# Optimization experiments

Measured on AMD Instinct MI355X. Metric: run time of the kernel, lower is better.

Reference implementation:

```python
import jax, jax.numpy as jnp
import numpy as np


def setup_inputs() -> dict:
    key = jax.random.key(0)
    k1, k2 = jax.random.split(key)
    B, H, W, D = 4096, 64, 64, 512
    inputs = jax.random.normal(k1, (B, D), dtype=jnp.float32)
    # keras 'random_uniform' initializer default range [-0.05, 0.05]
    weights_map = jax.random.uniform(k2, (H, W, D), dtype=jnp.float32,
                                     minval=-0.05, maxval=0.05)
    return {"inputs": inputs, "weights_map": weights_map}


def reference(inputs, weights_map):
    # inputs: (B, D); weights_map: (H, W, D)
    H, W, D = weights_map.shape
    flat_w = weights_map.reshape(-1, D)              # (N, D), N = H*W
    # avoids materializing the (B, N, D) difference tensor)
    x_sq = jnp.sum(inputs * inputs, axis=1, keepdims=True)    # (B, 1)
    w_sq = jnp.sum(flat_w * flat_w, axis=1)                   # (N,)
    sq_dist = x_sq - 2.0 * (inputs @ flat_w.T) + w_sq         # (B, N)
    sq_dist = jnp.maximum(sq_dist, 0.0)
    bmu_flat = jnp.argmin(sq_dist, axis=1)                    # (B,)
    bmu_y = (bmu_flat // W).astype(jnp.int32)
    bmu_x = (bmu_flat % W).astype(jnp.int32)
    bmu_indices = jnp.stack([bmu_y, bmu_x], axis=1)           # (B, 2)
    min_sq = jnp.take_along_axis(sq_dist, bmu_flat[:, None], axis=1)[:, 0]
    quantization_errors = jnp.sqrt(min_sq)                    # (B,)
    return bmu_indices, quantization_errors
```

## Files before the change

### kernel.cpp

```cpp
#include <hip/hip_runtime.h>

#define B_ROWS 4096
#define N_COLS 4096
#define DIM    512
#define LDK    1024

typedef __attribute__((ext_vector_type(8))) short short8;
typedef __attribute__((ext_vector_type(4))) float floatx4;

__device__ __forceinline__ unsigned short f2bf_rn(float f) {
    unsigned u = __float_as_uint(f);
    u += 0x7fffu + ((u >> 16) & 1u);
    return (unsigned short)(u >> 16);
}
__device__ __forceinline__ float bf2f(unsigned short h) {
    return __uint_as_float(((unsigned)h) << 16);
}

__device__ __forceinline__ unsigned long long pack_key(float v, int idx) {
    unsigned u = __float_as_uint(v);
    u = (u & 0x80000000u) ? ~u : (u | 0x80000000u);
    return ((unsigned long long)u << 32) | (unsigned)idx;
}

__device__ __forceinline__ void async16(const unsigned short* g, unsigned short* l) {
    __builtin_amdgcn_global_load_lds(
        (__attribute__((address_space(1))) void*)g,
        (__attribute__((address_space(3))) void*)l, 16, 0, 0);
}

__global__ __launch_bounds__(256) void som_convert(
    const float* __restrict__ X, const float* __restrict__ Wt,
    unsigned short* __restrict__ Xc, unsigned short* __restrict__ Wc,
    float* __restrict__ x_sq, float* __restrict__ w_sq,
    unsigned long long* __restrict__ packed)
{
    int wave = threadIdx.x >> 6, lane = threadIdx.x & 63;
    int grow = blockIdx.x * 4 + wave;
    bool isX = grow < B_ROWS;
    const float* src = isX ? (X + (size_t)grow * DIM)
                           : (Wt + (size_t)(grow - B_ROWS) * DIM);
    const float4* p4 = (const float4*)src;
    float4 a = p4[lane * 2], b = p4[lane * 2 + 1];
    float f[8] = {a.x, a.y, a.z, a.w, b.x, b.y, b.z, b.w};
    unsigned short hi[8], lo[8];
    float s = 0.f;
    #pragma unroll
    for (int t = 0; t < 8; ++t) {
        hi[t] = f2bf_rn(f[t]);
        lo[t] = f2bf_rn(f[t] - bf2f(hi[t]));
        s = fmaf(f[t], f[t], s);
    }
    unsigned short* dst = (isX ? Xc + (size_t)grow * LDK
                               : Wc + (size_t)(grow - B_ROWS) * LDK) + lane * 8;
    *(ushort4*)(dst)       = make_ushort4(hi[0], hi[1], hi[2], hi[3]);
    *(ushort4*)(dst + 4)   = make_ushort4(hi[4], hi[5], hi[6], hi[7]);
    *(ushort4*)(dst + 512) = make_ushort4(lo[0], lo[1], lo[2], lo[3]);
    *(ushort4*)(dst + 516) = make_ushort4(lo[4], lo[5], lo[6], lo[7]);
    #pragma unroll
    for (int off = 32; off >= 1; off >>= 1) s += __shfl_xor(s, off, 64);
    if (lane == 0) {
        if (isX) { x_sq[grow] = s; packed[grow] = ~0ull; }
        else     { w_sq[grow - B_ROWS] = s; }
    }
}

__global__ __launch_bounds__(256, 3) void som_dist_bf16(
    const unsigned short* __restrict__ Xc, const unsigned short* __restrict__ Wc,
    const float* __restrict__ w_sq, unsigned long long* __restrict__ packed)
{
    __shared__ unsigned short Ah[128 * 32];
    __shared__ unsigned short Al[128 * 32];
    __shared__ unsigned short Bh[128 * 32];
    __shared__ unsigned short Bl[128 * 32];
    const int tid  = threadIdx.x;
    const int wave = tid >> 6, lane = tid & 63;
    const int wr = wave >> 1, wc = wave & 1;
    const int bm = blockIdx.y, bn = blockIdx.x;
    const int quad = lane >> 4, t16 = lane & 15;

    const int srow = lane >> 2;
    const int scol = (lane & 3) * 8;
    const unsigned short* gAh = Xc + (size_t)(bm * 128 + wave * 32 + srow) * LDK + scol;
    const unsigned short* gBh = Wc + (size_t)(bn * 128 + wave * 32 + srow) * LDK + scol;
    const unsigned short* gAl = gAh + 512;
    const unsigned short* gBl = gBh + 512;
    unsigned short* lAh = &Ah[(wave * 32) * 32];
    unsigned short* lAl = &Al[(wave * 32) * 32];
    unsigned short* lBh = &Bh[(wave * 32) * 32];
    unsigned short* lBl = &Bl[(wave * 32) * 32];

    const unsigned short* pah = &Ah[(wr * 64 + t16) * 32 + quad * 8];
    const unsigned short* pal = &Al[(wr * 64 + t16) * 32 + quad * 8];
    const unsigned short* pbh = &Bh[(wc * 64 + t16) * 32 + quad * 8];
    const unsigned short* pbl = &Bl[(wc * 64 + t16) * 32 + quad * 8];

    floatx4 acc[4][4];
    #pragma unroll
    for (int i = 0; i < 4; ++i)
        #pragma unroll
        for (int j = 0; j < 4; ++j) acc[i][j] = (floatx4){0.f, 0.f, 0.f, 0.f};

    #pragma unroll 1
    for (int k0 = 0; k0 < DIM; k0 += 32) {
        __syncthreads();
        async16(gAh + k0,            lAh);
        async16(gAh + k0 + 16 * LDK, lAh + 16 * 32);
        async16(gAl + k0,            lAl);
        async16(gAl + k0 + 16 * LDK, lAl + 16 * 32);
        async16(gBh + k0,            lBh);
        async16(gBh + k0 + 16 * LDK, lBh + 16 * 32);
        async16(gBl + k0,            lBl);
        async16(gBl + k0 + 16 * LDK, lBl + 16 * 32);
        __syncthreads();

        short8 ah[4], bh[4], x[4];
        #pragma unroll
        for (int i = 0; i < 4; ++i) ah[i] = *(const short8*)(pah + i * 16 * 32);
        #pragma unroll
        for (int j = 0; j < 4; ++j) bh[j] = *(const short8*)(pbh + j * 16 * 32);
        #pragma unroll
        for (int i = 0; i < 4; ++i)
            #pragma unroll
            for (int j = 0; j < 4; ++j)
                acc[i][j] = __builtin_amdgcn_mfma_f32_16x16x32_bf16(
                    ah[i], bh[j], acc[i][j], 0, 0, 0);

        #pragma unroll
        for (int j = 0; j < 4; ++j) x[j] = *(const short8*)(pbl + j * 16 * 32);
        #pragma unroll
        for (int i = 0; i < 4; ++i)
            #pragma unroll
            for (int j = 0; j < 4; ++j)
                acc[i][j] = __builtin_amdgcn_mfma_f32_16x16x32_bf16(
                    ah[i], x[j], acc[i][j], 0, 0, 0);

        #pragma unroll
        for (int i = 0; i < 4; ++i) x[i] = *(const short8*)(pal + i * 16 * 32);
        #pragma unroll
        for (int i = 0; i < 4; ++i)
            #pragma unroll
            for (int j = 0; j < 4; ++j)
                acc[i][j] = __builtin_amdgcn_mfma_f32_16x16x32_bf16(
                    x[i], bh[j], acc[i][j], 0, 0, 0);
    }

    const int col0 = bn * 128 + wc * 64 + t16;
    float wq[4];
    #pragma unroll
    for (int j = 0; j < 4; ++j) wq[j] = w_sq[col0 + j * 16];
    const int row_base = bm * 128 + wr * 64 + quad * 4;
    #pragma unroll
    for (int i = 0; i < 4; ++i) {
        #pragma unroll
        for (int r = 0; r < 4; ++r) {
            unsigned long long best = ~0ull;
            #pragma unroll
            for (int j = 0; j < 4; ++j) {
                float val = fmaf(-2.f, acc[i][j][r], wq[j]);
                unsigned long long key = pack_key(val, col0 + j * 16);
                best = (key < best) ? key : best;
            }
            #pragma unroll
            for (int m = 1; m <= 8; m <<= 1) {
                unsigned long long o = __shfl_xor(best, m, 64);
                best = (o < best) ? o : best;
            }
            if (t16 == 0)
                atomicMin(&packed[row_base + i * 16 + r], best);
        }
    }
}

__global__ __launch_bounds__(256) void som_finalize(
    const unsigned long long* __restrict__ packed,
    const float* __restrict__ x_sq, float* __restrict__ out)
{
    int b = blockIdx.x * 256 + threadIdx.x;
    unsigned long long p = packed[b];
    unsigned idx = (unsigned)(p & 0xffffffffull);
    unsigned key = (unsigned)(p >> 32);
    unsigned u = (key & 0x80000000u) ? (key & 0x7fffffffu) : ~key;
    float val = __uint_as_float(u);
    float sq = fmaxf(x_sq[b] + val, 0.f);
    out[2 * b]     = (float)(idx >> 6);
    out[2 * b + 1] = (float)(idx & 63);
    out[2 * B_ROWS + b] = sqrtf(sq);
}

extern "C" void kernel_launch(void* const* d_in, const int* in_sizes, int n_in,
                              void* d_out, int out_size, void* d_ws, size_t ws_size,
                              hipStream_t stream) {
    const float* X  = (const float*)d_in[0];
    const float* Wt = (const float*)d_in[1];
    float* out = (float*)d_out;

    unsigned long long* packed = (unsigned long long*)d_ws;
    float* x_sq = (float*)((char*)d_ws + (32 << 10));
    float* w_sq = (float*)((char*)d_ws + (48 << 10));
    unsigned short* Xc = (unsigned short*)((char*)d_ws + (64 << 10));
    unsigned short* Wc = (unsigned short*)((char*)d_ws + (64 << 10) + ((size_t)B_ROWS * LDK * 2));

    som_convert<<<dim3((B_ROWS + N_COLS) / 4), dim3(256), 0, stream>>>(
        X, Wt, Xc, Wc, x_sq, w_sq, packed);
    som_dist_bf16<<<dim3(N_COLS / 128, B_ROWS / 128), dim3(256), 0, stream>>>(
        Xc, Wc, w_sq, packed);
    som_finalize<<<dim3(B_ROWS / 256), dim3(256), 0, stream>>>(packed, x_sq, out);
}
```

Baseline: 124.3 us.

## Enlarge GEMM tile to 256x256 with double-buffered LDS and 8 waves

Replaces the 128x128, 4-wave distance GEMM with a 256x256 block tile run by 8 waves, each owning a 128x64 output sub-tile. LDS is double-buffered, so global-to-LDS async loads for the next K slice overlap MFMA work on the current one, with one barrier per iteration instead of two. Raising MFMA priority with s_setprio is meant to favour compute issue. The costs are more accumulator registers (128 floats per lane), 128 KB of LDS per block, and only 256 blocks in the grid, which may leave some CUs idle or lower occupancy.

```diff
diff --git a/kernel.cpp b/kernel.cpp
--- a/kernel.cpp
+++ b/kernel.cpp
@@ -65,93 +65,103 @@
     }
 }
 
-__global__ __launch_bounds__(256, 3) void som_dist_bf16(
+__global__ __launch_bounds__(512, 2) void som_dist_v2(
     const unsigned short* __restrict__ Xc, const unsigned short* __restrict__ Wc,
     const float* __restrict__ w_sq, unsigned long long* __restrict__ packed)
 {
-    __shared__ unsigned short Ah[128 * 32];
-    __shared__ unsigned short Al[128 * 32];
-    __shared__ unsigned short Bh[128 * 32];
-    __shared__ unsigned short Bl[128 * 32];
+    __shared__ __align__(16) unsigned short L[2 * 64 * 512];
     const int tid  = threadIdx.x;
     const int wave = tid >> 6, lane = tid & 63;
-    const int wr = wave >> 1, wc = wave & 1;
+    const int quad = lane >> 4, t16 = lane & 15;
+    const int wr = wave >> 2, wc = wave & 3;
     const int bm = blockIdx.y, bn = blockIdx.x;
-    const int quad = lane >> 4, t16 = lane & 15;
-
-    const int srow = lane >> 2;
-    const int scol = (lane & 3) * 8;
-    const unsigned short* gAh = Xc + (size_t)(bm * 128 + wave * 32 + srow) * LDK + scol;
-    const unsigned short* gBh = Wc + (size_t)(bn * 128 + wave * 32 + srow) * LDK + scol;
-    const unsigned short* gAl = gAh + 512;
-    const unsigned short* gBl = gBh + 512;
-    unsigned short* lAh = &Ah[(wave * 32) * 32];
-    unsigned short* lAl = &Al[(wave * 32) * 32];
-    unsigned short* lBh = &Bh[(wave * 32) * 32];
-    unsigned short* lBl = &Bl[(wave * 32) * 32];
-
-    const unsigned short* pah = &Ah[(wr * 64 + t16) * 32 + quad * 8];
-    const unsigned short* pal = &Al[(wr * 64 + t16) * 32 + quad * 8];
-    const unsigned short* pbh = &Bh[(wc * 64 + t16) * 32 + quad * 8];
-    const unsigned short* pbl = &Bl[(wc * 64 + t16) * 32 + quad * 8];
-
-    floatx4 acc[4][4];
-    #pragma unroll
-    for (int i = 0; i < 4; ++i)
+
+    const int sg = wave & 3;
+    const bool stB = (wave >= 4);
+    const unsigned short* gsrc =
+        (stB ? Wc + (size_t)bn * 256 * LDK : Xc + (size_t)bm * 256 * LDK)
+        + (size_t)(sg * 64 + t16) * LDK + quad * 8;
+    unsigned short* const lwav = &L[(stB ? 16384 : 0) + sg * 4096];
+
+    const unsigned short* const pA = &L[wr * 8192 + lane * 8];
+    const unsigned short* const pB = &L[16384 + wc * 4096 + lane * 8];
+
+    floatx4 acc[8][4];
+    #pragma unroll
+    for (int i = 0; i < 8; ++i)
         #pragma unroll
         for (int j = 0; j < 4; ++j) acc[i][j] = (floatx4){0.f, 0.f, 0.f, 0.f};
 
-    #pragma unroll 1
-    for (int k0 = 0; k0 < DIM; k0 += 32) {
-        __syncthreads();
-        async16(gAh + k0,            lAh);
-        async16(gAh + k0 + 16 * LDK, lAh + 16 * 32);
-        async16(gAl + k0,            lAl);
-        async16(gAl + k0 + 16 * LDK, lAl + 16 * 32);
-        async16(gBh + k0,            lBh);
-        async16(gBh + k0 + 16 * LDK, lBh + 16 * 32);
-        async16(gBl + k0,            lBl);
-        async16(gBl + k0 + 16 * LDK, lBl + 16 * 32);
-        __syncthreads();
-
-        short8 ah[4], bh[4], x[4];
-        #pragma unroll
-        for (int i = 0; i < 4; ++i) ah[i] = *(const short8*)(pah + i * 16 * 32);
-        #pragma unroll
-        for (int j = 0; j < 4; ++j) bh[j] = *(const short8*)(pbh + j * 16 * 32);
-        #pragma unroll
-        for (int i = 0; i < 4; ++i)
+    #pragma unroll
+    for (int q = 0; q < 4; ++q) {
+        async16(gsrc + q * 16 * LDK,       lwav + q * 1024);
+        async16(gsrc + q * 16 * LDK + 512, lwav + q * 1024 + 512);
+    }
+    __syncthreads();
+
+    #pragma unroll 2
+    for (int kt = 0; kt < 16; ++kt) {
+        const int cur = kt & 1;
+        const unsigned short* pAc = pA + cur * 32768;
+        const unsigned short* pBc = pB + cur * 32768;
+
+        if (kt < 15) {
+            const unsigned short* gs = gsrc + (kt + 1) * 32;
+            unsigned short* ld = lwav + (cur ^ 1) * 32768;
+            #pragma unroll
+            for (int q = 0; q < 4; ++q) {
+                async16(gs + q * 16 * LDK,       ld + q * 1024);
+                async16(gs + q * 16 * LDK + 512, ld + q * 1024 + 512);
+            }
+        }
+
+        short8 ah[8], bh[4], x4[4];
+        #pragma unroll
+        for (int i = 0; i < 8; ++i) ah[i] = *(const short8*)(pAc + i * 1024);
+        #pragma unroll
+        for (int j = 0; j < 4; ++j) bh[j] = *(const short8*)(pBc + j * 1024);
+        __builtin_amdgcn_s_setprio(1);
+        #pragma unroll
+        for (int i = 0; i < 8; ++i)
             #pragma unroll
             for (int j = 0; j < 4; ++j)
                 acc[i][j] = __builtin_amdgcn_mfma_f32_16x16x32_bf16(
                     ah[i], bh[j], acc[i][j], 0, 0, 0);
-
-        #pragma unroll
-        for (int j = 0; j < 4; ++j) x[j] = *(const short8*)(pbl + j * 16 * 32);
-        #pragma unroll
-        for (int i = 0; i < 4; ++i)
+        __builtin_amdgcn_s_setprio(0);
+
+        #pragma unroll
+        for (int j = 0; j < 4; ++j) x4[j] = *(const short8*)(pBc + j * 1024 + 512);
+        __builtin_amdgcn_s_setprio(1);
+        #pragma unroll
+        for (int i = 0; i < 8; ++i)
             #pragma unroll
             for (int j = 0; j < 4; ++j)
                 acc[i][j] = __builtin_amdgcn_mfma_f32_16x16x32_bf16(
-                    ah[i], x[j], acc[i][j], 0, 0, 0);
-
-        #pragma unroll
-        for (int i = 0; i < 4; ++i) x[i] = *(const short8*)(pal + i * 16 * 32);
-        #pragma unroll
-        for (int i = 0; i < 4; ++i)
+                    ah[i], x4[j], acc[i][j], 0, 0, 0);
+        __builtin_amdgcn_s_setprio(0);
+
+        short8 al[8];
+        #pragma unroll
+        for (int i = 0; i < 8; ++i) al[i] = *(const short8*)(pAc + i * 1024 + 512);
+        __builtin_amdgcn_s_setprio(1);
+        #pragma unroll
+        for (int i = 0; i < 8; ++i)
             #pragma unroll
             for (int j = 0; j < 4; ++j)
                 acc[i][j] = __builtin_amdgcn_mfma_f32_16x16x32_bf16(
-                    x[i], bh[j], acc[i][j], 0, 0, 0);
-    }
-
-    const int col0 = bn * 128 + wc * 64 + t16;
+                    al[i], bh[j], acc[i][j], 0, 0, 0);
+        __builtin_amdgcn_s_setprio(0);
+
+        __syncthreads();
+    }
+
+    const int col0 = bn * 256 + wc * 64 + t16;
     float wq[4];
     #pragma unroll
     for (int j = 0; j < 4; ++j) wq[j] = w_sq[col0 + j * 16];
-    const int row_base = bm * 128 + wr * 64 + quad * 4;
-    #pragma unroll
-    for (int i = 0; i < 4; ++i) {
+    const int row_base = bm * 256 + wr * 128 + quad * 4;
+    #pragma unroll
+    for (int i = 0; i < 8; ++i) {
         #pragma unroll
         for (int r = 0; r < 4; ++r) {
             unsigned long long best = ~0ull;
@@ -203,7 +213,7 @@
 
     som_convert<<<dim3((B_ROWS + N_COLS) / 4), dim3(256), 0, stream>>>(
         X, Wt, Xc, Wc, x_sq, w_sq, packed);
-    som_dist_bf16<<<dim3(N_COLS / 128, B_ROWS / 128), dim3(256), 0, stream>>>(
+    som_dist_v2<<<dim3(N_COLS / 256, B_ROWS / 256), dim3(512), 0, stream>>>(
         Xc, Wc, w_sq, packed);
     som_finalize<<<dim3(B_ROWS / 256), dim3(256), 0, stream>>>(packed, x_sq, out);
 }
```

After: 118.7 us. -4.5%, faster.

## Reorganize LDS tile layout, remap blocks per XCD, widen convert stores

Applied to the files above, without the earlier changes.

The LDS tiles are laid out so that each MFMA operand fragment sits contiguously per lane (lane*8). This aims to cut bank conflicts on the short8 LDS reads. Global-to-LDS loads are split so waves 0-1 stage X and waves 2-3 stage W, with hi and lo halves interleaved per fragment. Block IDs are remapped so that blocks sharing an XCD work on neighbouring bm/bn tiles, improving L2 reuse. The convert kernel now writes 16-byte short8 stores instead of 8-byte ones.

```diff
diff --git a/kernel.cpp b/kernel.cpp
--- a/kernel.cpp
+++ b/kernel.cpp
@@ -43,20 +43,19 @@
     const float4* p4 = (const float4*)src;
     float4 a = p4[lane * 2], b = p4[lane * 2 + 1];
     float f[8] = {a.x, a.y, a.z, a.w, b.x, b.y, b.z, b.w};
-    unsigned short hi[8], lo[8];
+    short8 hi, lo;
     float s = 0.f;
     #pragma unroll
     for (int t = 0; t < 8; ++t) {
-        hi[t] = f2bf_rn(f[t]);
-        lo[t] = f2bf_rn(f[t] - bf2f(hi[t]));
+        unsigned short h = f2bf_rn(f[t]);
+        hi[t] = (short)h;
+        lo[t] = (short)f2bf_rn(f[t] - bf2f(h));
         s = fmaf(f[t], f[t], s);
     }
     unsigned short* dst = (isX ? Xc + (size_t)grow * LDK
                                : Wc + (size_t)(grow - B_ROWS) * LDK) + lane * 8;
-    *(ushort4*)(dst)       = make_ushort4(hi[0], hi[1], hi[2], hi[3]);
-    *(ushort4*)(dst + 4)   = make_ushort4(hi[4], hi[5], hi[6], hi[7]);
-    *(ushort4*)(dst + 512) = make_ushort4(lo[0], lo[1], lo[2], lo[3]);
-    *(ushort4*)(dst + 516) = make_ushort4(lo[4], lo[5], lo[6], lo[7]);
+    *(short8*)(dst)       = hi;
+    *(short8*)(dst + 512) = lo;
     #pragma unroll
     for (int off = 32; off >= 1; off >>= 1) s += __shfl_xor(s, off, 64);
     if (lane == 0) {
@@ -65,35 +64,31 @@
     }
 }
 
-__global__ __launch_bounds__(256, 3) void som_dist_bf16(
+__global__ __launch_bounds__(256, 3) void som_dist_v6(
     const unsigned short* __restrict__ Xc, const unsigned short* __restrict__ Wc,
     const float* __restrict__ w_sq, unsigned long long* __restrict__ packed)
 {
-    __shared__ unsigned short Ah[128 * 32];
-    __shared__ unsigned short Al[128 * 32];
-    __shared__ unsigned short Bh[128 * 32];
-    __shared__ unsigned short Bl[128 * 32];
+    __shared__ __align__(16) unsigned short L[16384];
     const int tid  = threadIdx.x;
     const int wave = tid >> 6, lane = tid & 63;
+    const int quad = lane >> 4, t16 = lane & 15;
     const int wr = wave >> 1, wc = wave & 1;
-    const int bm = blockIdx.y, bn = blockIdx.x;
-    const int quad = lane >> 4, t16 = lane & 15;
-
-    const int srow = lane >> 2;
-    const int scol = (lane & 3) * 8;
-    const unsigned short* gAh = Xc + (size_t)(bm * 128 + wave * 32 + srow) * LDK + scol;
-    const unsigned short* gBh = Wc + (size_t)(bn * 128 + wave * 32 + srow) * LDK + scol;
-    const unsigned short* gAl = gAh + 512;
-    const unsigned short* gBl = gBh + 512;
-    unsigned short* lAh = &Ah[(wave * 32) * 32];
-    unsigned short* lAl = &Al[(wave * 32) * 32];
-    unsigned short* lBh = &Bh[(wave * 32) * 32];
-    unsigned short* lBl = &Bl[(wave * 32) * 32];
-
-    const unsigned short* pah = &Ah[(wr * 64 + t16) * 32 + quad * 8];
-    const unsigned short* pal = &Al[(wr * 64 + t16) * 32 + quad * 8];
-    const unsigned short* pbh = &Bh[(wc * 64 + t16) * 32 + quad * 8];
-    const unsigned short* pbl = &Bl[(wc * 64 + t16) * 32 + quad * 8];
+
+    const int bid = blockIdx.y * 32 + blockIdx.x;
+    const int xcd = bid & 7, wix = bid >> 3;
+    const int bm = (xcd >> 2) * 16 + (wix & 15);
+    const int bn = (xcd & 3) * 8 + (wix >> 4);
+
+    const int sg = wave & 1;
+    const bool stB = (wave >= 2);
+    const unsigned short* gsrc =
+        (stB ? Wc + (size_t)bn * 128 * LDK : Xc + (size_t)bm * 128 * LDK)
+        + (size_t)(sg * 64 + t16) * LDK + quad * 8;
+    unsigned short* const lhi = &L[(stB ? 8192 : 0) + sg * 2048];
+    unsigned short* const llo = lhi + 4096;
+
+    const unsigned short* const pA = &L[wr * 2048 + lane * 8];
+    const unsigned short* const pB = &L[8192 + wc * 2048 + lane * 8];
 
     floatx4 acc[4][4];
     #pragma unroll
@@ -104,21 +99,18 @@
     #pragma unroll 1
     for (int k0 = 0; k0 < DIM; k0 += 32) {
         __syncthreads();
-        async16(gAh + k0,            lAh);
-        async16(gAh + k0 + 16 * LDK, lAh + 16 * 32);
-        async16(gAl + k0,            lAl);
-        async16(gAl + k0 + 16 * LDK, lAl + 16 * 32);
-        async16(gBh + k0,            lBh);
-        async16(gBh + k0 + 16 * LDK, lBh + 16 * 32);
-        async16(gBl + k0,            lBl);
-        async16(gBl + k0 + 16 * LDK, lBl + 16 * 32);
+        #pragma unroll
+        for (int q = 0; q < 4; ++q) {
+            async16(gsrc + k0 + q * 16 * LDK,       lhi + q * 512);
+            async16(gsrc + k0 + q * 16 * LDK + 512, llo + q * 512);
+        }
         __syncthreads();
 
         short8 ah[4], bh[4], x[4];
         #pragma unroll
-        for (int i = 0; i < 4; ++i) ah[i] = *(const short8*)(pah + i * 16 * 32);
-        #pragma unroll
-        for (int j = 0; j < 4; ++j) bh[j] = *(const short8*)(pbh + j * 16 * 32);
+        for (int i = 0; i < 4; ++i) ah[i] = *(const short8*)(pA + i * 512);
+        #pragma unroll
+        for (int j = 0; j < 4; ++j) bh[j] = *(const short8*)(pB + j * 512);
         #pragma unroll
         for (int i = 0; i < 4; ++i)
             #pragma unroll
@@ -127,7 +119,7 @@
                     ah[i], bh[j], acc[i][j], 0, 0, 0);
 
         #pragma unroll
-        for (int j = 0; j < 4; ++j) x[j] = *(const short8*)(pbl + j * 16 * 32);
+        for (int j = 0; j < 4; ++j) x[j] = *(const short8*)(pB + j * 512 + 4096);
         #pragma unroll
         for (int i = 0; i < 4; ++i)
             #pragma unroll
@@ -136,7 +128,7 @@
                     ah[i], x[j], acc[i][j], 0, 0, 0);
 
         #pragma unroll
-        for (int i = 0; i < 4; ++i) x[i] = *(const short8*)(pal + i * 16 * 32);
+        for (int i = 0; i < 4; ++i) x[i] = *(const short8*)(pA + i * 512 + 4096);
         #pragma unroll
         for (int i = 0; i < 4; ++i)
             #pragma unroll
@@ -203,7 +195,7 @@
 
     som_convert<<<dim3((B_ROWS + N_COLS) / 4), dim3(256), 0, stream>>>(
         X, Wt, Xc, Wc, x_sq, w_sq, packed);
-    som_dist_bf16<<<dim3(N_COLS / 128, B_ROWS / 128), dim3(256), 0, stream>>>(
+    som_dist_v6<<<dim3(32, 32), dim3(256), 0, stream>>>(
         Xc, Wc, w_sq, packed);
     som_finalize<<<dim3(B_ROWS / 256), dim3(256), 0, stream>>>(packed, x_sq, out);
 }
```

After: 137.9 us. 1.11x slower.
